# Optimization experiments

Measured on AMD Instinct MI355X. Metric: run time of the kernel, lower is better.

The kernel has to match this reference:

```python
import jax, jax.numpy as jnp
import numpy as np

HEAD = 8  # number of attention heads (init kwarg)


def setup_inputs() -> dict:
    key = jax.random.key(0)
    k1, k2, k3 = jax.random.split(key, 3)
    b, H, W, c = 8, 32, 32, 512
    dim = 512
    x = jax.random.normal(k1, (b, H, W, c), dtype=jnp.float32)
    # 1x1 Conv == per-pixel matmul over channels
    w_qkv = jax.random.normal(k2, (c, 3 * dim), dtype=jnp.float32) * (c ** -0.5)
    w_out = jax.random.normal(k3, (dim, dim), dtype=jnp.float32) * (dim ** -0.5)
    b_out = jnp.zeros((dim,), dtype=jnp.float32)
    return {"x": x, "w_qkv": w_qkv, "w_out": w_out, "b_out": b_out}


def reference(x, w_qkv, w_out, b_out):
    b, H, W, c = x.shape
    n = H * W
    # QKV 1x1-conv projection (no bias)
    qkv = jnp.einsum('bhwc,cd->bhwd', x, w_qkv)          # (b, H, W, 3*dim)
    qkv = qkv.reshape(b, n, HEAD, -1)                     # (b, n, head, 3*dh)
    q, k, v = jnp.split(qkv, 3, axis=-1)                  # each (b, n, head, dh)
    scale = b ** -0.5  # NOTE: source scales by batch size, reproduced faithfully
    attn = jax.nn.softmax(jnp.einsum('bihd,bjhd->bhij', q, k) * scale, axis=-1)
    out = jnp.einsum('bhij,bjhd->bihd', attn, v)          # (b, n, head, dh)
    out = out.reshape(b, H, W, -1)                        # (b, H, W, dim)
    # output 1x1-conv projection (with bias)
    return jnp.einsum('bhwc,cd->bhwd', out, w_out) + b_out
```

## Files before the change

kernel.cpp:

```cpp
#include <hip/hip_runtime.h>
#include <hip/hip_bf16.h>

typedef __bf16 bf16x8_t __attribute__((ext_vector_type(8)));
typedef float  f32x4_t  __attribute__((ext_vector_type(4)));
typedef short  s16x4_t  __attribute__((ext_vector_type(4)));
typedef short  s16x8_t  __attribute__((ext_vector_type(8)));

#define NTOK   1024
#define CDIM   512
#define QKVDIM 1536
#define NHEAD  8
#define DHEAD  64
#define C1EXP  0.51007088f
#define C2EXP  34.624681f

__device__ __forceinline__ float b2f(short s) {
    unsigned int u = ((unsigned int)(unsigned short)s) << 16;
    float f; __builtin_memcpy(&f, &u, 4); return f;
}
__device__ __forceinline__ short f2b(float f) {
    __bf16 h = (__bf16)f; short s; __builtin_memcpy(&s, &h, 2); return s;
}

__global__ __launch_bounds__(256) void cvt_w(
    const float* __restrict__ wq, const float* __restrict__ wo,
    short* __restrict__ wqbT, short* __restrict__ wobT)
{
    const int b = blockIdx.x;
    const int t = threadIdx.x;
    const int kk = t & 63, grp = t >> 6;
    if (b < 192) {
        const int K0 = (b & 7) * 64, N0 = (b >> 3) * 64;
#pragma unroll
        for (int s = 0; s < 16; ++s) {
            int n = N0 + grp * 16 + s;
            wqbT[(size_t)n * 512 + K0 + kk] = f2b(wq[(size_t)(K0 + kk) * 1536 + n]);
        }
    } else {
        const int b2 = b - 192;
        const int K0 = (b2 & 7) * 64, N0 = (b2 >> 3) * 64;
#pragma unroll
        for (int s = 0; s < 16; ++s) {
            int n = N0 + grp * 16 + s;
            wobT[(size_t)n * 512 + K0 + kk] = f2b(wo[(size_t)(K0 + kk) * 512 + n]);
        }
    }
}

__global__ __launch_bounds__(256) void gemm_qkv(
    const float* __restrict__ X, const short* __restrict__ Bt,
    short* __restrict__ qk, short* __restrict__ vT)
{
    __shared__ __align__(16) short Al[128 * 64];
    __shared__ __align__(16) short Bl[128 * 64];

    const int t = threadIdx.x;
    const int bid = blockIdx.x;
    const int xcd = bid & 7, jpos = bid >> 3;
    const int tm = xcd * 8 + jpos / 12;
    const int tn = jpos % 12;
    const int N0 = tn * 128, M0 = tm * 128;
    const int w = t >> 6, lane = t & 63;
    const int quad = lane >> 4, mr = lane & 15;
    const int wm = (w >> 1) * 64, wn = (w & 1) * 64;

    int srow[4], soff[4];
#pragma unroll
    for (int r = 0; r < 4; ++r) {
        int ci = r * 256 + t;
        srow[r] = ci >> 3;
        soff[r] = (ci & 7) * 8;
    }
    const float* Ag = X  + (size_t)M0 * 512;
    const short* Bg = Bt + (size_t)N0 * 512;

    float4  fa[4][2];
    s16x8_t br[4];
#pragma unroll
    for (int r = 0; r < 4; ++r) {
        const float* pa = Ag + (size_t)srow[r] * 512 + soff[r];
        fa[r][0] = *(const float4*)pa;
        fa[r][1] = *(const float4*)(pa + 4);
        br[r] = *(const s16x8_t*)(Bg + (size_t)srow[r] * 512 + soff[r]);
    }

    f32x4_t acc[4][4];
#pragma unroll
    for (int ms = 0; ms < 4; ++ms)
#pragma unroll
        for (int ns = 0; ns < 4; ++ns) acc[ms][ns] = f32x4_t{0.f,0.f,0.f,0.f};

#pragma unroll 1
    for (int kc = 0; kc < 8; ++kc) {
        __syncthreads();
#pragma unroll
        for (int r = 0; r < 4; ++r) {
            int lds = srow[r] * 64 + (((soff[r] >> 3) ^ (srow[r] & 7)) * 8);
            s16x8_t va;
            va[0] = f2b(fa[r][0].x); va[1] = f2b(fa[r][0].y);
            va[2] = f2b(fa[r][0].z); va[3] = f2b(fa[r][0].w);
            va[4] = f2b(fa[r][1].x); va[5] = f2b(fa[r][1].y);
            va[6] = f2b(fa[r][1].z); va[7] = f2b(fa[r][1].w);
            *(s16x8_t*)(Al + lds) = va;
            *(s16x8_t*)(Bl + lds) = br[r];
        }
        __syncthreads();
        if (kc < 7) {
            int k0 = (kc + 1) * 64;
#pragma unroll
            for (int r = 0; r < 4; ++r) {
                const float* pa = Ag + (size_t)srow[r] * 512 + k0 + soff[r];
                fa[r][0] = *(const float4*)pa;
                fa[r][1] = *(const float4*)(pa + 4);
                br[r] = *(const s16x8_t*)(Bg + (size_t)srow[r] * 512 + k0 + soff[r]);
            }
        }
#pragma unroll
        for (int kh = 0; kh < 2; ++kh) {
            bf16x8_t af[4], bf[4];
#pragma unroll
            for (int ms = 0; ms < 4; ++ms) {
                int rr = wm + ms * 16 + mr;
                af[ms] = *(const bf16x8_t*)(Al + rr * 64 + (((kh * 4 + quad) ^ (rr & 7)) * 8));
            }
#pragma unroll
            for (int ns = 0; ns < 4; ++ns) {
                int rr = wn + ns * 16 + mr;
                bf[ns] = *(const bf16x8_t*)(Bl + rr * 64 + (((kh * 4 + quad) ^ (rr & 7)) * 8));
            }
#pragma unroll
            for (int ms = 0; ms < 4; ++ms)
#pragma unroll
                for (int ns = 0; ns < 4; ++ns)
                    acc[ms][ns] = __builtin_amdgcn_mfma_f32_16x16x32_bf16(
                        af[ms], bf[ns], acc[ms][ns], 0, 0, 0);
        }
    }

#pragma unroll
    for (int ms = 0; ms < 4; ++ms) {
        int row = M0 + wm + ms * 16 + quad * 4;
        int bb = row >> 10, ti = row & 1023;
#pragma unroll
        for (int ns = 0; ns < 4; ++ns) {
            int c0 = N0 + wn + ns * 16;
            int hh = c0 / 192, r0 = c0 % 192;
            if (r0 < 128) {
                size_t base = (size_t)row * 1024 + hh * 128 + r0 + mr;
#pragma unroll
                for (int i = 0; i < 4; ++i)
                    qk[base + (size_t)i * 1024] = f2b(acc[ms][ns][i]);
            } else {
                s16x4_t v4;
#pragma unroll
                for (int i = 0; i < 4; ++i) v4[i] = f2b(acc[ms][ns][i]);
                *(s16x4_t*)(vT + ((size_t)(bb * 8 + hh) * 64 + (r0 - 128) + mr) * 1024 + ti) = v4;
            }
        }
    }
}

template <int N, bool BIAS, bool OUTF32>
__global__ __launch_bounds__(256) void gemm128(
    const short* __restrict__ A, const short* __restrict__ Bt,
    const float* __restrict__ bias, void* __restrict__ C)
{
    __shared__ __align__(16) short Al[128 * 64];
    __shared__ __align__(16) short Bl[128 * 64];

    constexpr int TNT = N / 128;
    const int t = threadIdx.x;
    const int bid = blockIdx.x;
    const int xcd = bid & 7, jpos = bid >> 3;
    const int tm = xcd * 8 + jpos / TNT;
    const int tn = jpos % TNT;
    const int N0 = tn * 128, M0 = tm * 128;
    const int w = t >> 6, lane = t & 63;
    const int quad = lane >> 4, mr = lane & 15;
    const int wm = (w >> 1) * 64, wn = (w & 1) * 64;

    int srow[4], soff[4];
#pragma unroll
    for (int r = 0; r < 4; ++r) {
        int ci = r * 256 + t;
        srow[r] = ci >> 3;
        soff[r] = (ci & 7) * 8;
    }
    const short* Ag = A  + (size_t)M0 * 512;
    const short* Bg = Bt + (size_t)N0 * 512;

    s16x8_t ar[4], br[4];
#pragma unroll
    for (int r = 0; r < 4; ++r) {
        ar[r] = *(const s16x8_t*)(Ag + (size_t)srow[r] * 512 + soff[r]);
        br[r] = *(const s16x8_t*)(Bg + (size_t)srow[r] * 512 + soff[r]);
    }

    f32x4_t acc[4][4];
#pragma unroll
    for (int ms = 0; ms < 4; ++ms)
#pragma unroll
        for (int ns = 0; ns < 4; ++ns) acc[ms][ns] = f32x4_t{0.f,0.f,0.f,0.f};

#pragma unroll 1
    for (int kc = 0; kc < 8; ++kc) {
        __syncthreads();
#pragma unroll
        for (int r = 0; r < 4; ++r) {
            int lds = srow[r] * 64 + (((soff[r] >> 3) ^ (srow[r] & 7)) * 8);
            *(s16x8_t*)(Al + lds) = ar[r];
            *(s16x8_t*)(Bl + lds) = br[r];
        }
        __syncthreads();
        if (kc < 7) {
            int k0 = (kc + 1) * 64;
#pragma unroll
            for (int r = 0; r < 4; ++r) {
                ar[r] = *(const s16x8_t*)(Ag + (size_t)srow[r] * 512 + k0 + soff[r]);
                br[r] = *(const s16x8_t*)(Bg + (size_t)srow[r] * 512 + k0 + soff[r]);
            }
        }
#pragma unroll
        for (int kh = 0; kh < 2; ++kh) {
            bf16x8_t af[4], bf[4];
#pragma unroll
            for (int ms = 0; ms < 4; ++ms) {
                int rr = wm + ms * 16 + mr;
                af[ms] = *(const bf16x8_t*)(Al + rr * 64 + (((kh * 4 + quad) ^ (rr & 7)) * 8));
            }
#pragma unroll
            for (int ns = 0; ns < 4; ++ns) {
                int rr = wn + ns * 16 + mr;
                bf[ns] = *(const bf16x8_t*)(Bl + rr * 64 + (((kh * 4 + quad) ^ (rr & 7)) * 8));
            }
#pragma unroll
            for (int ms = 0; ms < 4; ++ms)
#pragma unroll
                for (int ns = 0; ns < 4; ++ns)
                    acc[ms][ns] = __builtin_amdgcn_mfma_f32_16x16x32_bf16(
                        af[ms], bf[ns], acc[ms][ns], 0, 0, 0);
        }
    }

#pragma unroll
    for (int ms = 0; ms < 4; ++ms) {
        int row = M0 + wm + ms * 16 + quad * 4;
#pragma unroll
        for (int ns = 0; ns < 4; ++ns) {
            int col = N0 + wn + ns * 16 + mr;
            float bz = BIAS ? bias[col] : 0.f;
#pragma unroll
            for (int i = 0; i < 4; ++i) {
                if constexpr (OUTF32)
                    ((float*)C)[(size_t)(row + i) * N + col] = acc[ms][ns][i] + bz;
                else
                    ((short*)C)[(size_t)(row + i) * N + col] = f2b(acc[ms][ns][i]);
            }
        }
    }
}

__global__ __launch_bounds__(512, 2) void attn_st(
    const short* __restrict__ qk, const short* __restrict__ vT,
    short* __restrict__ aout)
{
    __shared__ __align__(16) short Kl[128 * 72];
    __shared__ __align__(16) short Vt[64 * 136];
    __shared__ __align__(16) short Pl[8][32 * 136];

    const int t = threadIdx.x;
    const int g = blockIdx.x;
    const int qt = (g >> 3) & 3;
    const int h = g & 7, b = g >> 5;
    const int w = t >> 6, lane = t & 63;
    const int quad = lane >> 4, mr = lane & 15;

    const size_t qra = (size_t)(b * NTOK + qt * 256 + w * 32 + mr) * 1024 + h * 128;
    const size_t qrb = qra + (size_t)16 * 1024;
    const bf16x8_t qf0a = *(const bf16x8_t*)(qk + qra + quad * 8);
    const bf16x8_t qf1a = *(const bf16x8_t*)(qk + qra + 32 + quad * 8);
    const bf16x8_t qf0b = *(const bf16x8_t*)(qk + qrb + quad * 8);
    const bf16x8_t qf1b = *(const bf16x8_t*)(qk + qrb + 32 + quad * 8);

    s16x8_t ones_s;
#pragma unroll
    for (int e = 0; e < 8; ++e) ones_s[e] = 0x3F80;
    const bf16x8_t onesv = *(const bf16x8_t*)&ones_s;

    f32x4_t L4a = f32x4_t{0.f,0.f,0.f,0.f}, L4b = f32x4_t{0.f,0.f,0.f,0.f};
    f32x4_t Oa[4], Ob[4];
#pragma unroll
    for (int d = 0; d < 4; ++d) {
        Oa[d] = f32x4_t{0.f,0.f,0.f,0.f};
        Ob[d] = f32x4_t{0.f,0.f,0.f,0.f};
    }

    short* Pma = Pl[w];
    short* Pmb = Pma + 16 * 136;

    const int kr0 = t >> 3, kr1 = kr0 + 64;
    const int kc8 = (t & 7) * 8;
    const int vr0 = t >> 4, vr1 = vr0 + 32;
    const int vc8 = (t & 15) * 8;

    const size_t kg = (size_t)(b * NTOK) * 1024 + h * 128 + 64 + kc8;
    const size_t vg = (size_t)(b * 8 + h) * 64 * 1024 + vc8;

    s16x8_t k0r, k1r, v0r, v1r;
    k0r = *(const s16x8_t*)(qk + kg + (size_t)kr0 * 1024);
    k1r = *(const s16x8_t*)(qk + kg + (size_t)kr1 * 1024);
    v0r = *(const s16x8_t*)(vT + vg + (size_t)vr0 * 1024);
    v1r = *(const s16x8_t*)(vT + vg + (size_t)vr1 * 1024);

#pragma unroll 1
    for (int jt = 0; jt < 8; ++jt) {
        *(s16x8_t*)(Kl + kr0 * 72 + kc8)  = k0r;
        *(s16x8_t*)(Kl + kr1 * 72 + kc8)  = k1r;
        *(s16x8_t*)(Vt + vr0 * 136 + vc8) = v0r;
        *(s16x8_t*)(Vt + vr1 * 136 + vc8) = v1r;
        __syncthreads();

        if (jt < 7) {
            int j0n = (jt + 1) * 128;
            k0r = *(const s16x8_t*)(qk + kg + (size_t)(j0n + kr0) * 1024);
            k1r = *(const s16x8_t*)(qk + kg + (size_t)(j0n + kr1) * 1024);
            v0r = *(const s16x8_t*)(vT + vg + (size_t)vr0 * 1024 + j0n);
            v1r = *(const s16x8_t*)(vT + vg + (size_t)vr1 * 1024 + j0n);
        }

#pragma unroll
        for (int jj = 0; jj < 8; ++jj) {
            const short* kb = Kl + (jj * 16 + mr) * 72 + quad * 8;
            const bf16x8_t kf0 = *(const bf16x8_t*)kb;
            const bf16x8_t kf1 = *(const bf16x8_t*)(kb + 32);
            __builtin_amdgcn_s_setprio(1);
            f32x4_t a0a = __builtin_amdgcn_mfma_f32_16x16x32_bf16(
                kf0, qf0a, f32x4_t{0.f,0.f,0.f,0.f}, 0, 0, 0);
            f32x4_t sa = __builtin_amdgcn_mfma_f32_16x16x32_bf16(
                kf1, qf1a, a0a, 0, 0, 0);
            f32x4_t a0b = __builtin_amdgcn_mfma_f32_16x16x32_bf16(
                kf0, qf0b, f32x4_t{0.f,0.f,0.f,0.f}, 0, 0, 0);
            f32x4_t sb = __builtin_amdgcn_mfma_f32_16x16x32_bf16(
                kf1, qf1b, a0b, 0, 0, 0);
            __builtin_amdgcn_s_setprio(0);
            s16x4_t pva, pvb;
#pragma unroll
            for (int r = 0; r < 4; ++r) {
                pva[r] = f2b(__builtin_amdgcn_exp2f(sa[r] * C1EXP - C2EXP));
                pvb[r] = f2b(__builtin_amdgcn_exp2f(sb[r] * C1EXP - C2EXP));
            }
            *(s16x4_t*)(Pma + mr * 136 + jj * 16 + quad * 4) = pva;
            *(s16x4_t*)(Pmb + mr * 136 + jj * 16 + quad * 4) = pvb;
        }

        bf16x8_t paa[4], pab[4];
#pragma unroll
        for (int ks = 0; ks < 4; ++ks) {
            paa[ks] = *(const bf16x8_t*)(Pma + mr * 136 + ks * 32 + quad * 8);
            pab[ks] = *(const bf16x8_t*)(Pmb + mr * 136 + ks * 32 + quad * 8);
        }

        __builtin_amdgcn_s_setprio(1);
#pragma unroll
        for (int ks = 0; ks < 4; ++ks) {
            L4a = __builtin_amdgcn_mfma_f32_16x16x32_bf16(paa[ks], onesv, L4a, 0, 0, 0);
            L4b = __builtin_amdgcn_mfma_f32_16x16x32_bf16(pab[ks], onesv, L4b, 0, 0, 0);
        }
#pragma unroll
        for (int dt = 0; dt < 4; ++dt) {
            const short* vb = Vt + (dt * 16 + mr) * 136 + quad * 8;
#pragma unroll
            for (int ks = 0; ks < 4; ++ks) {
                const bf16x8_t vf = *(const bf16x8_t*)(vb + ks * 32);
                Oa[dt] = __builtin_amdgcn_mfma_f32_16x16x32_bf16(paa[ks], vf, Oa[dt], 0, 0, 0);
                Ob[dt] = __builtin_amdgcn_mfma_f32_16x16x32_bf16(pab[ks], vf, Ob[dt], 0, 0, 0);
            }
        }
        __builtin_amdgcn_s_setprio(0);
        __syncthreads();
    }

#pragma unroll
    for (int dt = 0; dt < 4; ++dt)
#pragma unroll
        for (int i = 0; i < 4; ++i) {
            Pma[(quad * 4 + i) * 136 + dt * 16 + mr] = f2b(Oa[dt][i] * (1.f / L4a[i]));
            Pmb[(quad * 4 + i) * 136 + dt * 16 + mr] = f2b(Ob[dt][i] * (1.f / L4b[i]));
        }
    __syncthreads();

    const int q2 = lane >> 2, h2 = lane & 3;
#pragma unroll
    for (int it = 0; it < 2; ++it) {
        const int row = it * 16 + q2;
        const size_t tok = (size_t)(b * NTOK + qt * 256 + w * 32 + row);
        s16x8_t o0 = *(const s16x8_t*)(Pma + row * 136 + h2 * 16);
        s16x8_t o1 = *(const s16x8_t*)(Pma + row * 136 + h2 * 16 + 8);
        *(s16x8_t*)(aout + tok * CDIM + h * DHEAD + h2 * 16)     = o0;
        *(s16x8_t*)(aout + tok * CDIM + h * DHEAD + h2 * 16 + 8) = o1;
    }
}

extern "C" void kernel_launch(void* const* d_in, const int* in_sizes, int n_in,
                              void* d_out, int out_size, void* d_ws, size_t ws_size,
                              hipStream_t stream)
{
    const float* x     = (const float*)d_in[0];
    const float* w_qkv = (const float*)d_in[1];
    const float* w_out = (const float*)d_in[2];
    const float* b_out = (const float*)d_in[3];
    for (int i = 0; i < n_in; ++i) {
        if      (in_sizes[i] == 4194304) x     = (const float*)d_in[i];
        else if (in_sizes[i] ==  786432) w_qkv = (const float*)d_in[i];
        else if (in_sizes[i] ==  262144) w_out = (const float*)d_in[i];
        else if (in_sizes[i] ==     512) b_out = (const float*)d_in[i];
    }

    short* qk   = (short*)d_ws;
    short* vT   = (short*)((char*)d_ws + (size_t)8192 * 1024 * 2);
    short* aout = (short*)((char*)d_ws + (size_t)8192 * 1024 * 2 + (size_t)64 * 64 * 1024 * 2);
    short* wobT = (short*)((char*)d_ws + (size_t)33 * 1024 * 1024 + (size_t)1664 * 1024);
    short* wqbT = (short*)d_out + (size_t)8192 * 512;

    cvt_w<<<256, 256, 0, stream>>>(w_qkv, w_out, wqbT, wobT);

    gemm_qkv<<<768, 256, 0, stream>>>(x, wqbT, qk, vT);

    attn_st<<<256, 512, 0, stream>>>(qk, vT, aout);

    gemm128<CDIM, true, true>
        <<<(CDIM / 128) * 64, 256, 0, stream>>>(aout, wobT, b_out, d_out);
}
```

Before: 131.6 us.

## Pre-convert X to bf16 and read GEMM/attention operands directly from global memory

Adds a bf16 conversion of x to the weight-conversion kernel, writing it into the output buffer as scratch. The QKV GEMM then loads MFMA fragments straight from global memory into registers with double buffering, with no LDS staging and no barriers, and gets an occupancy hint. The attention kernel likewise drops its K/V LDS tiles and per-tile barriers and reads K and V fragments from global memory. The aim is to remove LDS round-trips and synchronisation. The cost is an extra full pass over x and strided, less coalesced global loads that now depend on cache hits.

```diff
diff --git a/kernel.cpp b/kernel.cpp
--- a/kernel.cpp
+++ b/kernel.cpp
@@ -14,20 +14,28 @@
 #define C1EXP  0.51007088f
 #define C2EXP  34.624681f
 
-__device__ __forceinline__ float b2f(short s) {
-    unsigned int u = ((unsigned int)(unsigned short)s) << 16;
-    float f; __builtin_memcpy(&f, &u, 4); return f;
-}
 __device__ __forceinline__ short f2b(float f) {
     __bf16 h = (__bf16)f; short s; __builtin_memcpy(&s, &h, 2); return s;
 }
 
-__global__ __launch_bounds__(256) void cvt_w(
-    const float* __restrict__ wq, const float* __restrict__ wo,
+__global__ __launch_bounds__(256) void cvt_fused(
+    const float* __restrict__ x, const float* __restrict__ wq,
+    const float* __restrict__ wo, short* __restrict__ xb,
     short* __restrict__ wqbT, short* __restrict__ wobT)
 {
-    const int b = blockIdx.x;
+    const int bid = blockIdx.x;
     const int t = threadIdx.x;
+    if (bid < 2048) {
+        int i = bid * 256 + t;
+        const float* p = x + (size_t)i * 8;
+        float4 a = *(const float4*)p, b = *(const float4*)(p + 4);
+        s16x8_t v;
+        v[0]=f2b(a.x); v[1]=f2b(a.y); v[2]=f2b(a.z); v[3]=f2b(a.w);
+        v[4]=f2b(b.x); v[5]=f2b(b.y); v[6]=f2b(b.z); v[7]=f2b(b.w);
+        *(s16x8_t*)(xb + (size_t)i * 8) = v;
+        return;
+    }
+    const int b = bid - 2048;
     const int kk = t & 63, grp = t >> 6;
     if (b < 192) {
         const int K0 = (b & 7) * 64, N0 = (b >> 3) * 64;
@@ -47,13 +55,10 @@
     }
 }
 
-__global__ __launch_bounds__(256) void gemm_qkv(
-    const float* __restrict__ X, const short* __restrict__ Bt,
+__global__ __launch_bounds__(256, 3) void gemm_qkv(
+    const short* __restrict__ A, const short* __restrict__ Bt,
     short* __restrict__ qk, short* __restrict__ vT)
 {
-    __shared__ __align__(16) short Al[128 * 64];
-    __shared__ __align__(16) short Bl[128 * 64];
-
     const int t = threadIdx.x;
     const int bid = blockIdx.x;
     const int xcd = bid & 7, jpos = bid >> 3;
@@ -64,24 +69,12 @@
     const int quad = lane >> 4, mr = lane & 15;
     const int wm = (w >> 1) * 64, wn = (w & 1) * 64;
 
-    int srow[4], soff[4];
-#pragma unroll
-    for (int r = 0; r < 4; ++r) {
-        int ci = r * 256 + t;
-        srow[r] = ci >> 3;
-        soff[r] = (ci & 7) * 8;
-    }
-    const float* Ag = X  + (size_t)M0 * 512;
-    const short* Bg = Bt + (size_t)N0 * 512;
-
-    float4  fa[4][2];
-    s16x8_t br[4];
-#pragma unroll
-    for (int r = 0; r < 4; ++r) {
-        const float* pa = Ag + (size_t)srow[r] * 512 + soff[r];
-        fa[r][0] = *(const float4*)pa;
-        fa[r][1] = *(const float4*)(pa + 4);
-        br[r] = *(const s16x8_t*)(Bg + (size_t)srow[r] * 512 + soff[r]);
+    const short* pa[4];
+    const short* pb[4];
+#pragma unroll
+    for (int i = 0; i < 4; ++i) {
+        pa[i] = A  + (size_t)(M0 + wm + i * 16 + mr) * 512 + quad * 8;
+        pb[i] = Bt + (size_t)(N0 + wn + i * 16 + mr) * 512 + quad * 8;
     }
 
     f32x4_t acc[4][4];
@@ -90,51 +83,41 @@
 #pragma unroll
         for (int ns = 0; ns < 4; ++ns) acc[ms][ns] = f32x4_t{0.f,0.f,0.f,0.f};
 
+    auto domfma = [&](s16x8_t* AA, s16x8_t* BB) {
+#pragma unroll
+        for (int ms = 0; ms < 4; ++ms)
+#pragma unroll
+            for (int ns = 0; ns < 4; ++ns)
+                acc[ms][ns] = __builtin_amdgcn_mfma_f32_16x16x32_bf16(
+                    *(const bf16x8_t*)&AA[ms], *(const bf16x8_t*)&BB[ns],
+                    acc[ms][ns], 0, 0, 0);
+    };
+
+    s16x8_t a0[4], b0[4], a1[4], b1[4];
+#pragma unroll
+    for (int i = 0; i < 4; ++i) {
+        a0[i] = *(const s16x8_t*)(pa[i]);
+        b0[i] = *(const s16x8_t*)(pb[i]);
+    }
+
+    int ko = 0;
 #pragma unroll 1
-    for (int kc = 0; kc < 8; ++kc) {
-        __syncthreads();
-#pragma unroll
-        for (int r = 0; r < 4; ++r) {
-            int lds = srow[r] * 64 + (((soff[r] >> 3) ^ (srow[r] & 7)) * 8);
-            s16x8_t va;
-            va[0] = f2b(fa[r][0].x); va[1] = f2b(fa[r][0].y);
-            va[2] = f2b(fa[r][0].z); va[3] = f2b(fa[r][0].w);
-            va[4] = f2b(fa[r][1].x); va[5] = f2b(fa[r][1].y);
-            va[6] = f2b(fa[r][1].z); va[7] = f2b(fa[r][1].w);
-            *(s16x8_t*)(Al + lds) = va;
-            *(s16x8_t*)(Bl + lds) = br[r];
-        }
-        __syncthreads();
-        if (kc < 7) {
-            int k0 = (kc + 1) * 64;
-#pragma unroll
-            for (int r = 0; r < 4; ++r) {
-                const float* pa = Ag + (size_t)srow[r] * 512 + k0 + soff[r];
-                fa[r][0] = *(const float4*)pa;
-                fa[r][1] = *(const float4*)(pa + 4);
-                br[r] = *(const s16x8_t*)(Bg + (size_t)srow[r] * 512 + k0 + soff[r]);
-            }
-        }
-#pragma unroll
-        for (int kh = 0; kh < 2; ++kh) {
-            bf16x8_t af[4], bf[4];
-#pragma unroll
-            for (int ms = 0; ms < 4; ++ms) {
-                int rr = wm + ms * 16 + mr;
-                af[ms] = *(const bf16x8_t*)(Al + rr * 64 + (((kh * 4 + quad) ^ (rr & 7)) * 8));
-            }
-#pragma unroll
-            for (int ns = 0; ns < 4; ++ns) {
-                int rr = wn + ns * 16 + mr;
-                bf[ns] = *(const bf16x8_t*)(Bl + rr * 64 + (((kh * 4 + quad) ^ (rr & 7)) * 8));
-            }
-#pragma unroll
-            for (int ms = 0; ms < 4; ++ms)
-#pragma unroll
-                for (int ns = 0; ns < 4; ++ns)
-                    acc[ms][ns] = __builtin_amdgcn_mfma_f32_16x16x32_bf16(
-                        af[ms], bf[ns], acc[ms][ns], 0, 0, 0);
-        }
+    for (int s = 0; s < 8; ++s) {
+#pragma unroll
+        for (int i = 0; i < 4; ++i) {
+            a1[i] = *(const s16x8_t*)(pa[i] + ko + 32);
+            b1[i] = *(const s16x8_t*)(pb[i] + ko + 32);
+        }
+        domfma(a0, b0);
+        if (s < 7) {
+#pragma unroll
+            for (int i = 0; i < 4; ++i) {
+                a0[i] = *(const s16x8_t*)(pa[i] + ko + 64);
+                b0[i] = *(const s16x8_t*)(pb[i] + ko + 64);
+            }
+        }
+        domfma(a1, b1);
+        ko += 64;
     }
 
 #pragma unroll
@@ -264,8 +247,6 @@
     const short* __restrict__ qk, const short* __restrict__ vT,
     short* __restrict__ aout)
 {
-    __shared__ __align__(16) short Kl[128 * 72];
-    __shared__ __align__(16) short Vt[64 * 136];
     __shared__ __align__(16) short Pl[8][32 * 136];
 
     const int t = threadIdx.x;
@@ -298,41 +279,16 @@
     short* Pma = Pl[w];
     short* Pmb = Pma + 16 * 136;
 
-    const int kr0 = t >> 3, kr1 = kr0 + 64;
-    const int kc8 = (t & 7) * 8;
-    const int vr0 = t >> 4, vr1 = vr0 + 32;
-    const int vc8 = (t & 15) * 8;
-
-    const size_t kg = (size_t)(b * NTOK) * 1024 + h * 128 + 64 + kc8;
-    const size_t vg = (size_t)(b * 8 + h) * 64 * 1024 + vc8;
-
-    s16x8_t k0r, k1r, v0r, v1r;
-    k0r = *(const s16x8_t*)(qk + kg + (size_t)kr0 * 1024);
-    k1r = *(const s16x8_t*)(qk + kg + (size_t)kr1 * 1024);
-    v0r = *(const s16x8_t*)(vT + vg + (size_t)vr0 * 1024);
-    v1r = *(const s16x8_t*)(vT + vg + (size_t)vr1 * 1024);
+    const short* Kg = qk + (size_t)(b * NTOK) * 1024 + h * 128 + 64 + quad * 8;
+    const short* Vg = vT + (size_t)(b * 8 + h) * 65536 + quad * 8;
 
 #pragma unroll 1
     for (int jt = 0; jt < 8; ++jt) {
-        *(s16x8_t*)(Kl + kr0 * 72 + kc8)  = k0r;
-        *(s16x8_t*)(Kl + kr1 * 72 + kc8)  = k1r;
-        *(s16x8_t*)(Vt + vr0 * 136 + vc8) = v0r;
-        *(s16x8_t*)(Vt + vr1 * 136 + vc8) = v1r;
-        __syncthreads();
-
-        if (jt < 7) {
-            int j0n = (jt + 1) * 128;
-            k0r = *(const s16x8_t*)(qk + kg + (size_t)(j0n + kr0) * 1024);
-            k1r = *(const s16x8_t*)(qk + kg + (size_t)(j0n + kr1) * 1024);
-            v0r = *(const s16x8_t*)(vT + vg + (size_t)vr0 * 1024 + j0n);
-            v1r = *(const s16x8_t*)(vT + vg + (size_t)vr1 * 1024 + j0n);
-        }
-
 #pragma unroll
         for (int jj = 0; jj < 8; ++jj) {
-            const short* kb = Kl + (jj * 16 + mr) * 72 + quad * 8;
-            const bf16x8_t kf0 = *(const bf16x8_t*)kb;
-            const bf16x8_t kf1 = *(const bf16x8_t*)(kb + 32);
+            const short* kr = Kg + (size_t)(jt * 128 + jj * 16 + mr) * 1024;
+            const bf16x8_t kf0 = *(const bf16x8_t*)kr;
+            const bf16x8_t kf1 = *(const bf16x8_t*)(kr + 32);
             __builtin_amdgcn_s_setprio(1);
             f32x4_t a0a = __builtin_amdgcn_mfma_f32_16x16x32_bf16(
                 kf0, qf0a, f32x4_t{0.f,0.f,0.f,0.f}, 0, 0, 0);
@@ -368,16 +324,15 @@
         }
 #pragma unroll
         for (int dt = 0; dt < 4; ++dt) {
-            const short* vb = Vt + (dt * 16 + mr) * 136 + quad * 8;
+            const short* vrow = Vg + (size_t)(dt * 16 + mr) * 1024 + jt * 128;
 #pragma unroll
             for (int ks = 0; ks < 4; ++ks) {
-                const bf16x8_t vf = *(const bf16x8_t*)(vb + ks * 32);
+                const bf16x8_t vf = *(const bf16x8_t*)(vrow + ks * 32);
                 Oa[dt] = __builtin_amdgcn_mfma_f32_16x16x32_bf16(paa[ks], vf, Oa[dt], 0, 0, 0);
                 Ob[dt] = __builtin_amdgcn_mfma_f32_16x16x32_bf16(pab[ks], vf, Ob[dt], 0, 0, 0);
             }
         }
         __builtin_amdgcn_s_setprio(0);
-        __syncthreads();
     }
 
 #pragma unroll
@@ -420,11 +375,12 @@
     short* vT   = (short*)((char*)d_ws + (size_t)8192 * 1024 * 2);
     short* aout = (short*)((char*)d_ws + (size_t)8192 * 1024 * 2 + (size_t)64 * 64 * 1024 * 2);
     short* wobT = (short*)((char*)d_ws + (size_t)33 * 1024 * 1024 + (size_t)1664 * 1024);
+    short* xb   = (short*)d_out;
     short* wqbT = (short*)d_out + (size_t)8192 * 512;
 
-    cvt_w<<<256, 256, 0, stream>>>(w_qkv, w_out, wqbT, wobT);
-
-    gemm_qkv<<<768, 256, 0, stream>>>(x, wqbT, qk, vT);
+    cvt_fused<<<2304, 256, 0, stream>>>(x, w_qkv, w_out, xb, wqbT, wobT);
+
+    gemm_qkv<<<768, 256, 0, stream>>>(xb, wqbT, qk, vT);
 
     attn_st<<<256, 512, 0, stream>>>(qk, vT, aout);
 
```

Result: slower. 201.4 us (+53.1%).
